# Kernel tuning notes

Hardware: AMD Instinct MI355X
Metric: run time of the kernel (lower is better)

Reference implementation:

```python
import jax, jax.numpy as jnp
import numpy as np

N_INPUT, N_HIDDEN, N_OUTPUT = 64, 1024, 64
B, T = 128, 512

def setup_inputs() -> dict:
    key = jax.random.key(0)
    ks = jax.random.split(key, 8)
    s_in = 1.0 / np.sqrt(N_INPUT)
    s_h = 1.0 / np.sqrt(N_HIDDEN)
    return {
        "x": jax.random.normal(ks[0], (B, T, N_INPUT), jnp.float32),
        "enc_w": jax.random.uniform(ks[1], (N_HIDDEN, N_INPUT), jnp.float32, -s_in, s_in),
        "enc_b": jax.random.uniform(ks[2], (N_HIDDEN,), jnp.float32, -s_in, s_in),
        "rec_w": jax.random.uniform(ks[3], (N_HIDDEN, N_HIDDEN), jnp.float32, -s_h, s_h),
        "fgt_w": jax.random.uniform(ks[4], (N_HIDDEN, N_HIDDEN), jnp.float32, -s_h, s_h),
        "dec_w": jax.random.uniform(ks[5], (N_OUTPUT, N_HIDDEN), jnp.float32, -s_h, s_h),
        "dec_b": jax.random.uniform(ks[6], (N_OUTPUT,), jnp.float32, -s_h, s_h),
        "hinit_w": jax.random.uniform(ks[7], (N_HIDDEN, 1), jnp.float32, -1.0, 1.0),
        "hinit_b": jax.random.uniform(jax.random.fold_in(key, 9), (N_HIDDEN,), jnp.float32, -1.0, 1.0),
    }

def softsign(x):
    return x / (1.0 + jnp.abs(x))

def reference(x, enc_w, enc_b, rec_w, fgt_w, dec_w, dec_b, hinit_w, hinit_b):
    # x: [B, T, I] -> time-major [T, B, I]
    xt = jnp.transpose(x, (1, 0, 2))
    # hidden_init(ones(B,1)) = ones @ hinit_w^T + b = broadcast of column sum
    hidden0 = jnp.broadcast_to(hinit_w[:, 0] + hinit_b, (x.shape[0], hinit_b.shape[0]))
    # Precompute encoder projection for all timesteps (same math, one big GEMM)
    enc_all = jnp.einsum('tbi,hi->tbh', xt, enc_w) + enc_b  # [T, B, H]

    def step(hidden, enc_t):
        forget = jax.nn.sigmoid(hidden @ fgt_w.T)
        hidden_new = softsign(enc_t + hidden @ rec_w.T)
        hidden = (1.0 - forget) * hidden + forget * hidden_new
        out_t = hidden @ dec_w.T + dec_b
        return hidden, out_t

    hidden, output = jax.lax.scan(step, hidden0, enc_all)
    return output, hidden  # output: [T, B, O], hidden: [B, H]
```

## Files before the change

kernel.cpp:

```cpp
#include <hip/hip_runtime.h>

typedef unsigned short u16;

#define NWG 256
#define NT  256
#define TS  512
#define HD  1024
#define BS  128
#define NI  64
#define NO  64
#define XR  16
#define CC  32
#define RCP 17

typedef __attribute__((ext_vector_type(8))) short bf16x8;
typedef __attribute__((ext_vector_type(4))) float f32x4;

__device__ __forceinline__ float bf2f(u16 u) {
    union { unsigned int i; float f; } v; v.i = ((unsigned int)u) << 16; return v.f;
}
__device__ __forceinline__ u16 f2bf(float f) {
    union { float fl; unsigned int i; } v; v.fl = f;
    unsigned int x = v.i;
    return (u16)((x + 0x7fffu + ((x >> 16) & 1u)) >> 16);
}
__device__ __forceinline__ float ldv(const void* p, size_t i, bool isf32) {
    return isf32 ? ((const float*)p)[i] : bf2f(((const u16*)p)[i]);
}

__device__ __forceinline__ unsigned l2_atomic_add(unsigned* p, unsigned v) {
    unsigned old;
    asm volatile("global_atomic_add %0, %1, %2, off sc0\n\t"
                 "s_waitcnt vmcnt(0)"
                 : "=&v"(old) : "v"(p), "v"(v) : "memory");
    return old;
}

__device__ __forceinline__ void load_a_frags(const u16* ap, bf16x8* a) {
    asm volatile(
        "global_load_dwordx4 %0, %8, off sc0\n\t"
        "global_load_dwordx4 %1, %8, off offset:64 sc0\n\t"
        "global_load_dwordx4 %2, %8, off offset:128 sc0\n\t"
        "global_load_dwordx4 %3, %8, off offset:192 sc0\n\t"
        "global_load_dwordx4 %4, %8, off offset:256 sc0\n\t"
        "global_load_dwordx4 %5, %8, off offset:320 sc0\n\t"
        "global_load_dwordx4 %6, %8, off offset:384 sc0\n\t"
        "global_load_dwordx4 %7, %8, off offset:448 sc0\n\t"
        "s_waitcnt vmcnt(0)"
        : "=&v"(a[0]), "=&v"(a[1]), "=&v"(a[2]), "=&v"(a[3]),
          "=&v"(a[4]), "=&v"(a[5]), "=&v"(a[6]), "=&v"(a[7])
        : "v"(ap) : "memory");
}

#define CNT_STRIDE 16

__global__ __launch_bounds__(NT)
void arnn_xcd(const void* __restrict__ xv,
              const void* __restrict__ encwv,
              const void* __restrict__ encbv,
              const void* __restrict__ recwv,
              const void* __restrict__ fgtwv,
              const void* __restrict__ decwv,
              const void* __restrict__ decbv,
              const void* __restrict__ hinitwv,
              const void* __restrict__ hinitbv,
              void* __restrict__ outv,
              u16* __restrict__ h0buf,
              u16* __restrict__ h1buf,
              unsigned* __restrict__ tickets,
              unsigned* __restrict__ cnts)
{
    __shared__ short WB[132 * 64 * 8];
    __shared__ float redC[4 * 5 * 16 * RCP];
    __shared__ float hst[XR * CC];
    __shared__ float encbS[CC];
    __shared__ float decbLS[16];
    __shared__ unsigned s_xcd, s_slot;
    __shared__ int s_f32;

    const int tid  = threadIdx.x;
    const int wave = tid >> 6;
    const int lane = tid & 63;
    const int m    = lane & 15;
    const int quad = lane >> 4;

    if (tid == 0) {
        unsigned xcc;
        asm volatile("s_getreg_b32 %0, hwreg(HW_REG_XCC_ID, 0, 4)" : "=s"(xcc));
        xcc &= 7u;
        unsigned slot = l2_atomic_add(tickets + xcc * 16, 1u);
        s_xcd = xcc;
        s_slot = slot & 31u;
        s_f32 = 0;
    }
    __syncthreads();
    {
        float v = bf2f(((const u16*)recwv)[tid]);
        if (!(v >= -1.0f && v <= 1.0f)) s_f32 = 1;
    }
    __syncthreads();
    const bool isf32 = (s_f32 != 0);
    const int xcd  = (int)s_xcd;
    const int slot = (int)s_slot;
    const int b0   = xcd * XR;
    const int j0   = slot * CC;
    const int dt   = slot & 3;
    unsigned* qcnt = cnts + (size_t)xcd * 520 * CNT_STRIDE;

    for (int idx = tid; idx < 132 * 64; idx += NT) {
        int ksg = idx >> 6, l = idx & 63, n = l & 15, q = l >> 4;
        int tile, ksl;
        if (ksg < 34)       { tile = 0; ksl = ksg; }
        else if (ksg < 68)  { tile = 1; ksl = ksg - 34; }
        else if (ksg < 100) { tile = 2; ksl = ksg - 68; }
        else                { tile = 3; ksl = ksg - 100; }
        int j = j0 + ((tile & 1) << 4) + n;
        bf16x8 v;
        if (!isf32) {
            const u16* src;
            if (tile < 2) src = (ksl < 32) ? (const u16*)recwv + (size_t)j * HD + ksl * 32 + q * 8
                                           : (const u16*)encwv + (size_t)j * NI + (ksl - 32) * 32 + q * 8;
            else          src = (const u16*)fgtwv + (size_t)j * HD + ksl * 32 + q * 8;
            v = *(const bf16x8*)src;
        } else {
            const float* src;
            if (tile < 2) src = (ksl < 32) ? (const float*)recwv + (size_t)j * HD + ksl * 32 + q * 8
                                           : (const float*)encwv + (size_t)j * NI + (ksl - 32) * 32 + q * 8;
            else          src = (const float*)fgtwv + (size_t)j * HD + ksl * 32 + q * 8;
            #pragma unroll
            for (int i = 0; i < 8; ++i) v[i] = (short)f2bf(src[i]);
        }
        *(bf16x8*)&WB[idx * 8] = v;
    }
    __syncthreads();

    bf16x8 Breg[2][8];
    #pragma unroll
    for (int ks = 0; ks < 8; ++ks) {
        int kb = wave * 8 + ks;
        Breg[0][ks] = *(const bf16x8*)&WB[((0  + kb) * 64 + lane) * 8];
        Breg[1][ks] = *(const bf16x8*)&WB[((34 + kb) * 64 + lane) * 8];
    }
    bf16x8 Ereg[2];
    if (wave < 2) {
        Ereg[0] = *(const bf16x8*)&WB[((32 + wave) * 64 + lane) * 8];
        Ereg[1] = *(const bf16x8*)&WB[((34 + 32 + wave) * 64 + lane) * 8];
    }
    bf16x8 dfr[8];
    {
        int o = 16 * dt + m;
        #pragma unroll
        for (int ks = 0; ks < 8; ++ks) {
            int kb = wave * 256 + ks * 32 + quad * 8;
            if (!isf32) dfr[ks] = *(const bf16x8*)((const u16*)decwv + (size_t)o * HD + kb);
            else {
                const float* src = (const float*)decwv + (size_t)o * HD + kb;
                #pragma unroll
                for (int i = 0; i < 8; ++i) dfr[ks][i] = (short)f2bf(src[i]);
            }
        }
    }
    if (tid < CC) encbS[tid] = ldv(encbv, j0 + tid, isf32);
    if (tid < 16) decbLS[tid] = ldv(decbv, 16 * dt + tid, isf32);
    for (int e = tid; e < XR * CC; e += NT) {
        int r = e >> 5, c = e & 31;
        float v = ldv(hinitwv, j0 + c, isf32) + ldv(hinitbv, j0 + c, isf32);
        hst[e] = v;
        h0buf[(size_t)(b0 + r) * HD + j0 + c] = f2bf(v);
    }
    __syncthreads();
    if (tid == 0) l2_atomic_add(qcnt + 0 * CNT_STRIDE, 1u);

    for (int t = 0; t < TS; ++t) {
        f32x4 acc[5];
        #pragma unroll
        for (int tt = 0; tt < 5; ++tt) acc[tt] = (f32x4){0.f, 0.f, 0.f, 0.f};

        if (wave < 2) {
            bf16x8 xf;
            size_t xb = (size_t)(b0 + m) * (TS * NI) + (size_t)t * NI + wave * 32 + quad * 8;
            if (!isf32) xf = *(const bf16x8*)((const u16*)xv + xb);
            else {
                const float* xp = (const float*)xv + xb;
                #pragma unroll
                for (int i = 0; i < 8; ++i) xf[i] = (short)f2bf(xp[i]);
            }
            acc[0] = __builtin_amdgcn_mfma_f32_16x16x32_bf16(xf, Ereg[0], acc[0], 0, 0, 0);
            acc[1] = __builtin_amdgcn_mfma_f32_16x16x32_bf16(xf, Ereg[1], acc[1], 0, 0, 0);
        }

        if (wave == 0 && lane == 0) {
            unsigned* p = qcnt + (size_t)t * CNT_STRIDE;
            while (l2_atomic_add(p, 0u) < 32u) __builtin_amdgcn_s_sleep(1);
        }
        __syncthreads();

        const u16* cur = (t & 1) ? h1buf : h0buf;
        u16*       nxt = (t & 1) ? h0buf : h1buf;

        bf16x8 a[8];
        load_a_frags(cur + (size_t)(b0 + m) * HD + wave * 256 + quad * 8, a);

        #pragma unroll
        for (int ks = 0; ks < 8; ++ks) {
            int kb = wave * 8 + ks;
            bf16x8 bf2 = *(const bf16x8*)&WB[((68  + kb) * 64 + lane) * 8];
            bf16x8 bf3 = *(const bf16x8*)&WB[((100 + kb) * 64 + lane) * 8];
            acc[0] = __builtin_amdgcn_mfma_f32_16x16x32_bf16(a[ks], Breg[0][ks], acc[0], 0, 0, 0);
            acc[1] = __builtin_amdgcn_mfma_f32_16x16x32_bf16(a[ks], Breg[1][ks], acc[1], 0, 0, 0);
            acc[2] = __builtin_amdgcn_mfma_f32_16x16x32_bf16(a[ks], bf2,         acc[2], 0, 0, 0);
            acc[3] = __builtin_amdgcn_mfma_f32_16x16x32_bf16(a[ks], bf3,         acc[3], 0, 0, 0);
            acc[4] = __builtin_amdgcn_mfma_f32_16x16x32_bf16(a[ks], dfr[ks],     acc[4], 0, 0, 0);
        }

        #pragma unroll
        for (int tt = 0; tt < 5; ++tt) {
            #pragma unroll
            for (int r = 0; r < 4; ++r)
                redC[((wave * 5 + tt) * 16 + quad * 4 + r) * RCP + m] = acc[tt][r];
        }
        __syncthreads();

        for (int e = tid; e < XR * CC; e += NT) {
            int r = e >> 5, c = e & 31, tl = c >> 4, col = c & 15;
            float pr = encbS[c], pf = 0.f;
            #pragma unroll
            for (int kq = 0; kq < 4; ++kq) {
                pr += redC[((kq * 5 + tl) * 16 + r) * RCP + col];
                pf += redC[((kq * 5 + 2 + tl) * 16 + r) * RCP + col];
            }
            float fg = 1.0f / (1.0f + __expf(-pf));
            float hn = pr / (1.0f + fabsf(pr));
            float h  = hst[e];
            float hv = h + fg * (hn - h);
            hst[e] = hv;
            nxt[(size_t)(b0 + r) * HD + j0 + c] = f2bf(hv);
        }
        __syncthreads();
        if (tid == 0) l2_atomic_add(qcnt + (size_t)(t + 1) * CNT_STRIDE, 1u);

        if (slot < 4 && t > 0) {
            int r = tid >> 4, col = tid & 15;
            float o = decbLS[col];
            #pragma unroll
            for (int kq = 0; kq < 4; ++kq)
                o += redC[((kq * 5 + 4) * 16 + r) * RCP + col];
            size_t oi = (size_t)(t - 1) * (BS * NO) + (size_t)(b0 + r) * NO + 16 * dt + col;
            if (isf32) ((float*)outv)[oi] = o; else ((u16*)outv)[oi] = f2bf(o);
        }
    }

    if (wave == 0 && lane == 0) {
        unsigned* p = qcnt + (size_t)TS * CNT_STRIDE;
        while (l2_atomic_add(p, 0u) < 32u) __builtin_amdgcn_s_sleep(1);
    }
    __syncthreads();
    {
        bf16x8 a[8];
        load_a_frags(h0buf + (size_t)(b0 + m) * HD + wave * 256 + quad * 8, a);
        f32x4 ac = (f32x4){0.f, 0.f, 0.f, 0.f};
        #pragma unroll
        for (int ks = 0; ks < 8; ++ks)
            ac = __builtin_amdgcn_mfma_f32_16x16x32_bf16(a[ks], dfr[ks], ac, 0, 0, 0);
        #pragma unroll
        for (int r = 0; r < 4; ++r)
            redC[((wave * 5 + 4) * 16 + quad * 4 + r) * RCP + m] = ac[r];
        __syncthreads();
        if (slot < 4) {
            int r = tid >> 4, col = tid & 15;
            float o = decbLS[col];
            #pragma unroll
            for (int kq = 0; kq < 4; ++kq)
                o += redC[((kq * 5 + 4) * 16 + r) * RCP + col];
            size_t oi = (size_t)511 * (BS * NO) + (size_t)(b0 + r) * NO + 16 * dt + col;
            if (isf32) ((float*)outv)[oi] = o; else ((u16*)outv)[oi] = f2bf(o);
        }
        for (int e = tid; e < XR * CC; e += NT) {
            int r = e >> 5, c = e & 31;
            size_t oi = (size_t)TS * BS * NO + (size_t)(b0 + r) * HD + j0 + c;
            float v = hst[e];
            if (isf32) ((float*)outv)[oi] = v; else ((u16*)outv)[oi] = f2bf(v);
        }
    }
}

extern "C" void kernel_launch(void* const* d_in, const int* in_sizes, int n_in,
                              void* d_out, int out_size, void* d_ws, size_t ws_size,
                              hipStream_t stream) {
    (void)in_sizes; (void)n_in; (void)out_size; (void)ws_size;
    const void* xv       = d_in[0];
    const void* encwv    = d_in[1];
    const void* encbv    = d_in[2];
    const void* recwv    = d_in[3];
    const void* fgtwv    = d_in[4];
    const void* decwv    = d_in[5];
    const void* decbv    = d_in[6];
    const void* hinitwv  = d_in[7];
    const void* hinitbv  = d_in[8];
    void* outv = d_out;

    unsigned* tickets = (unsigned*)d_ws;
    unsigned* cnts    = (unsigned*)((char*)d_ws + 4096);
    u16* h0buf = (u16*)((char*)d_ws + 524288);
    u16* h1buf = h0buf + (size_t)BS * HD;

    hipMemsetAsync(d_ws, 0, 4096 + 8 * 520 * 64, stream);

    void* args[] = { (void*)&xv, (void*)&encwv, (void*)&encbv, (void*)&recwv,
                     (void*)&fgtwv, (void*)&decwv, (void*)&decbv,
                     (void*)&hinitwv, (void*)&hinitbv,
                     (void*)&outv, (void*)&h0buf, (void*)&h1buf,
                     (void*)&tickets, (void*)&cnts };
    hipError_t err = hipLaunchCooperativeKernel((void*)arnn_xcd, dim3(NWG), dim3(NT), args, 0, stream);
    if (err != hipSuccess) {
        hipLaunchKernelGGL(arnn_xcd, dim3(NWG), dim3(NT), 0, stream,
                           xv, encwv, encbv, recwv, fgtwv, decwv, decbv,
                           hinitwv, hinitbv, outv, h0buf, h1buf, tickets, cnts);
    }
}
```

Measured before the change: 1.627 ms.

## Replace per-step counter barrier with per-workgroup mailboxes and per-wave polling

Each workgroup now has its own mailbox counter per XCD group. Producers broadcast 32 fire-and-forget atomic increments, one per peer mailbox, instead of bumping a single shared per-step counter. Every wave polls its own workgroup's mailbox against a monotonically growing target, with no sleep and no __syncthreads, so polling is no longer funnelled through one thread. The decoder output write is moved ahead of the state update so the signal goes out sooner. This cuts contention on one hot atomic and removes a block barrier from the critical path, at the cost of 32 atomics per step and busy-wait traffic from four waves per workgroup.

```diff
diff --git a/kernel.cpp b/kernel.cpp
--- a/kernel.cpp
+++ b/kernel.cpp
@@ -34,6 +34,9 @@
                  "s_waitcnt vmcnt(0)"
                  : "=&v"(old) : "v"(p), "v"(v) : "memory");
     return old;
+}
+__device__ __forceinline__ void l2_atomic_add_nr(unsigned* p, unsigned v) {
+    asm volatile("global_atomic_add %0, %1, off" :: "v"(p), "v"(v) : "memory");
 }
 
 __device__ __forceinline__ void load_a_frags(const u16* ap, bf16x8* a) {
@@ -52,7 +55,7 @@
         : "v"(ap) : "memory");
 }
 
-#define CNT_STRIDE 16
+#define MB_STRIDE 16
 
 __global__ __launch_bounds__(NT)
 void arnn_xcd(const void* __restrict__ xv,
@@ -68,7 +71,7 @@
               u16* __restrict__ h0buf,
               u16* __restrict__ h1buf,
               unsigned* __restrict__ tickets,
-              unsigned* __restrict__ cnts)
+              unsigned* __restrict__ mboxes)
 {
     __shared__ short WB[132 * 64 * 8];
     __shared__ float redC[4 * 5 * 16 * RCP];
@@ -105,7 +108,8 @@
     const int b0   = xcd * XR;
     const int j0   = slot * CC;
     const int dt   = slot & 3;
-    unsigned* qcnt = cnts + (size_t)xcd * 520 * CNT_STRIDE;
+    unsigned* mbX   = mboxes + (size_t)xcd * 32 * MB_STRIDE;
+    unsigned* mbOwn = mbX + slot * MB_STRIDE;
 
     for (int idx = tid; idx < 132 * 64; idx += NT) {
         int ksg = idx >> 6, l = idx & 63, n = l & 15, q = l >> 4;
@@ -169,7 +173,7 @@
         h0buf[(size_t)(b0 + r) * HD + j0 + c] = f2bf(v);
     }
     __syncthreads();
-    if (tid == 0) l2_atomic_add(qcnt + 0 * CNT_STRIDE, 1u);
+    if (tid < 32) l2_atomic_add_nr(mbX + tid * MB_STRIDE, 1u);
 
     for (int t = 0; t < TS; ++t) {
         f32x4 acc[5];
@@ -189,11 +193,10 @@
             acc[1] = __builtin_amdgcn_mfma_f32_16x16x32_bf16(xf, Ereg[1], acc[1], 0, 0, 0);
         }
 
-        if (wave == 0 && lane == 0) {
-            unsigned* p = qcnt + (size_t)t * CNT_STRIDE;
-            while (l2_atomic_add(p, 0u) < 32u) __builtin_amdgcn_s_sleep(1);
-        }
-        __syncthreads();
+        if (lane == 0) {
+            unsigned target = 32u * (unsigned)(t + 1);
+            while (l2_atomic_add(mbOwn, 0u) < target) {}
+        }
 
         const u16* cur = (t & 1) ? h1buf : h0buf;
         u16*       nxt = (t & 1) ? h0buf : h1buf;
@@ -221,6 +224,15 @@
         }
         __syncthreads();
 
+        if (slot < 4 && t > 0) {
+            int r = tid >> 4, col = tid & 15;
+            float o = decbLS[col];
+            #pragma unroll
+            for (int kq = 0; kq < 4; ++kq)
+                o += redC[((kq * 5 + 4) * 16 + r) * RCP + col];
+            size_t oi = (size_t)(t - 1) * (BS * NO) + (size_t)(b0 + r) * NO + 16 * dt + col;
+            if (isf32) ((float*)outv)[oi] = o; else ((u16*)outv)[oi] = f2bf(o);
+        }
         for (int e = tid; e < XR * CC; e += NT) {
             int r = e >> 5, c = e & 31, tl = c >> 4, col = c & 15;
             float pr = encbS[c], pf = 0.f;
@@ -237,24 +249,13 @@
             nxt[(size_t)(b0 + r) * HD + j0 + c] = f2bf(hv);
         }
         __syncthreads();
-        if (tid == 0) l2_atomic_add(qcnt + (size_t)(t + 1) * CNT_STRIDE, 1u);
-
-        if (slot < 4 && t > 0) {
-            int r = tid >> 4, col = tid & 15;
-            float o = decbLS[col];
-            #pragma unroll
-            for (int kq = 0; kq < 4; ++kq)
-                o += redC[((kq * 5 + 4) * 16 + r) * RCP + col];
-            size_t oi = (size_t)(t - 1) * (BS * NO) + (size_t)(b0 + r) * NO + 16 * dt + col;
-            if (isf32) ((float*)outv)[oi] = o; else ((u16*)outv)[oi] = f2bf(o);
-        }
-    }
-
-    if (wave == 0 && lane == 0) {
-        unsigned* p = qcnt + (size_t)TS * CNT_STRIDE;
-        while (l2_atomic_add(p, 0u) < 32u) __builtin_amdgcn_s_sleep(1);
-    }
-    __syncthreads();
+        if (tid < 32) l2_atomic_add_nr(mbX + tid * MB_STRIDE, 1u);
+    }
+
+    if (lane == 0) {
+        unsigned target = 32u * (unsigned)(TS + 1);
+        while (l2_atomic_add(mbOwn, 0u) < target) {}
+    }
     {
         bf16x8 a[8];
         load_a_frags(h0buf + (size_t)(b0 + m) * HD + wave * 256 + quad * 8, a);
@@ -300,21 +301,21 @@
     void* outv = d_out;
 
     unsigned* tickets = (unsigned*)d_ws;
-    unsigned* cnts    = (unsigned*)((char*)d_ws + 4096);
+    unsigned* mboxes  = (unsigned*)((char*)d_ws + 4096);
     u16* h0buf = (u16*)((char*)d_ws + 524288);
     u16* h1buf = h0buf + (size_t)BS * HD;
 
-    hipMemsetAsync(d_ws, 0, 4096 + 8 * 520 * 64, stream);
+    hipMemsetAsync(d_ws, 0, 4096 + 8 * 32 * 64, stream);
 
     void* args[] = { (void*)&xv, (void*)&encwv, (void*)&encbv, (void*)&recwv,
                      (void*)&fgtwv, (void*)&decwv, (void*)&decbv,
                      (void*)&hinitwv, (void*)&hinitbv,
                      (void*)&outv, (void*)&h0buf, (void*)&h1buf,
-                     (void*)&tickets, (void*)&cnts };
+                     (void*)&tickets, (void*)&mboxes };
     hipError_t err = hipLaunchCooperativeKernel((void*)arnn_xcd, dim3(NWG), dim3(NT), args, 0, stream);
     if (err != hipSuccess) {
         hipLaunchKernelGGL(arnn_xcd, dim3(NWG), dim3(NT), 0, stream,
                            xv, encwv, encbv, recwv, fgtwv, decwv, decbv,
-                           hinitwv, hinitbv, outv, h0buf, h1buf, tickets, cnts);
-    }
-}
+                           hinitwv, hinitbv, outv, h0buf, h1buf, tickets, mboxes);
+    }
+}
```

Result: no change. 1.605 ms (-1.4%).

## Replace per-step atomic counters with per-block epoch flags polled by a full wave

Applied to the files above, without the earlier changes.

Each block now publishes progress by plainly storing an epoch number to its own flag, instead of doing an atomic increment on a shared per-step counter. All 32 lanes of wave 0 poll the 32 peer flags in parallel and use a wave vote to detect completion. The hidden-state update now has each thread handle two adjacent elements and write them as one packed 32-bit store, and the decoder output write is moved ahead of it. The aim is to cut atomic serialization and latency on the per-timestep barrier. The cost is heavier polling traffic, and correctness now depends on the non-atomic flag stores being visible through L2.

```diff
diff --git a/kernel.cpp b/kernel.cpp
--- a/kernel.cpp
+++ b/kernel.cpp
@@ -34,6 +34,9 @@
                  "s_waitcnt vmcnt(0)"
                  : "=&v"(old) : "v"(p), "v"(v) : "memory");
     return old;
+}
+__device__ __forceinline__ void l2_store_nr(unsigned* p, unsigned v) {
+    asm volatile("global_store_dword %0, %1, off sc0" :: "v"(p), "v"(v) : "memory");
 }
 
 __device__ __forceinline__ void load_a_frags(const u16* ap, bf16x8* a) {
@@ -52,7 +55,7 @@
         : "v"(ap) : "memory");
 }
 
-#define CNT_STRIDE 16
+#define FL_STRIDE 16
 
 __global__ __launch_bounds__(NT)
 void arnn_xcd(const void* __restrict__ xv,
@@ -68,7 +71,7 @@
               u16* __restrict__ h0buf,
               u16* __restrict__ h1buf,
               unsigned* __restrict__ tickets,
-              unsigned* __restrict__ cnts)
+              unsigned* __restrict__ flags)
 {
     __shared__ short WB[132 * 64 * 8];
     __shared__ float redC[4 * 5 * 16 * RCP];
@@ -105,7 +108,8 @@
     const int b0   = xcd * XR;
     const int j0   = slot * CC;
     const int dt   = slot & 3;
-    unsigned* qcnt = cnts + (size_t)xcd * 520 * CNT_STRIDE;
+    unsigned* flX   = flags + (size_t)xcd * 32 * FL_STRIDE;
+    unsigned* flOwn = flX + slot * FL_STRIDE;
 
     for (int idx = tid; idx < 132 * 64; idx += NT) {
         int ksg = idx >> 6, l = idx & 63, n = l & 15, q = l >> 4;
@@ -169,7 +173,7 @@
         h0buf[(size_t)(b0 + r) * HD + j0 + c] = f2bf(v);
     }
     __syncthreads();
-    if (tid == 0) l2_atomic_add(qcnt + 0 * CNT_STRIDE, 1u);
+    if (tid == 0) l2_store_nr(flOwn, 1u);
 
     for (int t = 0; t < TS; ++t) {
         f32x4 acc[5];
@@ -189,9 +193,13 @@
             acc[1] = __builtin_amdgcn_mfma_f32_16x16x32_bf16(xf, Ereg[1], acc[1], 0, 0, 0);
         }
 
-        if (wave == 0 && lane == 0) {
-            unsigned* p = qcnt + (size_t)t * CNT_STRIDE;
-            while (l2_atomic_add(p, 0u) < 32u) __builtin_amdgcn_s_sleep(1);
+        if (wave == 0) {
+            unsigned* p = flX + (lane & 31) * FL_STRIDE;
+            unsigned target = (unsigned)(t + 1);
+            for (;;) {
+                unsigned f = l2_atomic_add(p, 0u);
+                if (__all((int)(f >= target))) break;
+            }
         }
         __syncthreads();
 
@@ -221,24 +229,6 @@
         }
         __syncthreads();
 
-        for (int e = tid; e < XR * CC; e += NT) {
-            int r = e >> 5, c = e & 31, tl = c >> 4, col = c & 15;
-            float pr = encbS[c], pf = 0.f;
-            #pragma unroll
-            for (int kq = 0; kq < 4; ++kq) {
-                pr += redC[((kq * 5 + tl) * 16 + r) * RCP + col];
-                pf += redC[((kq * 5 + 2 + tl) * 16 + r) * RCP + col];
-            }
-            float fg = 1.0f / (1.0f + __expf(-pf));
-            float hn = pr / (1.0f + fabsf(pr));
-            float h  = hst[e];
-            float hv = h + fg * (hn - h);
-            hst[e] = hv;
-            nxt[(size_t)(b0 + r) * HD + j0 + c] = f2bf(hv);
-        }
-        __syncthreads();
-        if (tid == 0) l2_atomic_add(qcnt + (size_t)(t + 1) * CNT_STRIDE, 1u);
-
         if (slot < 4 && t > 0) {
             int r = tid >> 4, col = tid & 15;
             float o = decbLS[col];
@@ -248,11 +238,40 @@
             size_t oi = (size_t)(t - 1) * (BS * NO) + (size_t)(b0 + r) * NO + 16 * dt + col;
             if (isf32) ((float*)outv)[oi] = o; else ((u16*)outv)[oi] = f2bf(o);
         }
-    }
-
-    if (wave == 0 && lane == 0) {
-        unsigned* p = qcnt + (size_t)TS * CNT_STRIDE;
-        while (l2_atomic_add(p, 0u) < 32u) __builtin_amdgcn_s_sleep(1);
+        {
+            int e = tid * 2;
+            int r = e >> 5, c = e & 31, tl = c >> 4, col = c & 15;
+            float pr0 = encbS[c],     pf0 = 0.f;
+            float pr1 = encbS[c + 1], pf1 = 0.f;
+            #pragma unroll
+            for (int kq = 0; kq < 4; ++kq) {
+                pr0 += redC[((kq * 5 + tl) * 16 + r) * RCP + col];
+                pr1 += redC[((kq * 5 + tl) * 16 + r) * RCP + col + 1];
+                pf0 += redC[((kq * 5 + 2 + tl) * 16 + r) * RCP + col];
+                pf1 += redC[((kq * 5 + 2 + tl) * 16 + r) * RCP + col + 1];
+            }
+            float fg0 = 1.0f / (1.0f + __expf(-pf0));
+            float fg1 = 1.0f / (1.0f + __expf(-pf1));
+            float hn0 = pr0 / (1.0f + fabsf(pr0));
+            float hn1 = pr1 / (1.0f + fabsf(pr1));
+            float h0v = hst[e], h1v = hst[e + 1];
+            float hv0 = h0v + fg0 * (hn0 - h0v);
+            float hv1 = h1v + fg1 * (hn1 - h1v);
+            hst[e] = hv0; hst[e + 1] = hv1;
+            unsigned pk = (unsigned)f2bf(hv0) | ((unsigned)f2bf(hv1) << 16);
+            *(unsigned*)(nxt + (size_t)(b0 + r) * HD + j0 + c) = pk;
+        }
+        __syncthreads();
+        if (tid == 0) l2_store_nr(flOwn, (unsigned)(t + 2));
+    }
+
+    if (wave == 0) {
+        unsigned* p = flX + (lane & 31) * FL_STRIDE;
+        unsigned target = (unsigned)(TS + 1);
+        for (;;) {
+            unsigned f = l2_atomic_add(p, 0u);
+            if (__all((int)(f >= target))) break;
+        }
     }
     __syncthreads();
     {
@@ -300,21 +319,21 @@
     void* outv = d_out;
 
     unsigned* tickets = (unsigned*)d_ws;
-    unsigned* cnts    = (unsigned*)((char*)d_ws + 4096);
+    unsigned* flags   = (unsigned*)((char*)d_ws + 4096);
     u16* h0buf = (u16*)((char*)d_ws + 524288);
     u16* h1buf = h0buf + (size_t)BS * HD;
 
-    hipMemsetAsync(d_ws, 0, 4096 + 8 * 520 * 64, stream);
+    hipMemsetAsync(d_ws, 0, 4096 + 8 * 32 * 64, stream);
 
     void* args[] = { (void*)&xv, (void*)&encwv, (void*)&encbv, (void*)&recwv,
                      (void*)&fgtwv, (void*)&decwv, (void*)&decbv,
                      (void*)&hinitwv, (void*)&hinitbv,
                      (void*)&outv, (void*)&h0buf, (void*)&h1buf,
-                     (void*)&tickets, (void*)&cnts };
+                     (void*)&tickets, (void*)&flags };
     hipError_t err = hipLaunchCooperativeKernel((void*)arnn_xcd, dim3(NWG), dim3(NT), args, 0, stream);
     if (err != hipSuccess) {
         hipLaunchKernelGGL(arnn_xcd, dim3(NWG), dim3(NT), 0, stream,
                            xv, encwv, encbv, recwv, fgtwv, decwv, decbv,
-                           hinitwv, hinitbv, outv, h0buf, h1buf, tickets, cnts);
-    }
-}
+                           hinitwv, hinitbv, outv, h0buf, h1buf, tickets, flags);
+    }
+}
```

New measurement: 2.693 ms. 65.5% more time.
